# Kernel optimization log

Measured on AMD Instinct MI355X. Metric: run time of the kernel, lower is better.

The kernel has to match this reference:

```python
import jax, jax.numpy as jnp
import numpy as np

B = 16      # number of point clouds in the batch
N = 2048    # points per cloud
P = B * N   # total points (flat PyG-style batching)
K = 16      # neighbors per point (col 0 = self loop)
OUT = 512   # out_channels


def _linear(key, fi, fo):
    # torch nn.Linear default init: U(-1/sqrt(fi), 1/sqrt(fi))
    s = 1.0 / np.sqrt(fi)
    kw, kb = jax.random.split(key)
    W = jax.random.uniform(kw, (fi, fo), jnp.float32, -s, s)
    b = jax.random.uniform(kb, (fo,), jnp.float32, -s, s)
    return W, b


def setup_inputs() -> dict:
    key = jax.random.key(0)
    ks = jax.random.split(key, 6)
    pos = jax.random.normal(ks[0], (P, 3), jnp.float32)
    # flat batch vector: points are grouped contiguously per cloud
    batch = (jnp.arange(P, dtype=jnp.int32) // N).astype(jnp.int32)
    # within-cloud random neighbor indices (stand-in for knn/radius graph)
    base = (jnp.arange(P) // N) * N  # offset of each point's cloud
    nbr = base[:, None] + jax.random.randint(ks[1], (P, K), 0, N)
    nbr = nbr.at[:, 0].set(jnp.arange(P))  # self loop (PyG add_self_loops)
    W1, b1 = _linear(ks[2], 3, 64)          # sa1 MLP layer 1
    W2, b2 = _linear(ks[3], 64, 128)        # sa1 MLP layer 2
    W3, b3 = _linear(ks[4], 128 + 3, 256)   # sa2 MLP layer 1
    W4, b4 = _linear(ks[5], 256, OUT)       # sa2 MLP layer 2
    return dict(pos=pos, nbr=nbr.astype(jnp.int64), batch=batch,
                W1=W1, b1=b1, W2=W2, b2=b2, W3=W3, b3=b3, W4=W4, b4=b4)


def reference(pos, nbr, batch, W1, b1, W2, b2, W3, b3, W4, b4):
    # ----- sa1: x is None -> message = MLP(pos_j - pos_i), max-aggregated -----
    diff = pos[nbr] - pos[:, None, :]                      # [P, K, 3]
    h1 = jnp.maximum(diff @ W1 + b1, 0.0) @ W2 + b2        # [P, K, 128]
    x1 = jnp.max(h1, axis=1)                               # [P, 128]
    # ----- sa2: message = MLP([x1_j, pos_j - pos_i]), max-aggregated -----
    feats = jnp.concatenate([x1[nbr], diff], axis=-1)      # [P, K, 131]
    h2 = jnp.maximum(feats @ W3 + b3, 0.0) @ W4 + b4       # [P, K, 512]
    x2 = jnp.max(h2, axis=1)                               # [P, 512]
    # ----- global_max_pool over batch -----
    return jax.ops.segment_max(x2, batch, num_segments=B)  # [B, 512]
```

## Files before the change

kernel.cpp:

```cpp
#include <hip/hip_runtime.h>
#include <hip/hip_bf16.h>

#define PTOT   32768
#define KNB    16
#define NCLOUD 16
#define OUTC   512
#define A1S    168
#define A2S    264

typedef __attribute__((ext_vector_type(8)))  short v8bf;
typedef __attribute__((ext_vector_type(16))) float v16f;

__device__ __forceinline__ unsigned short f2b(float v) {
    __hip_bfloat16 h = __float2bfloat16(v);
    return *reinterpret_cast<unsigned short*>(&h);
}
__device__ __forceinline__ unsigned pk2(float a, float b) {
    return (unsigned)f2b(a) | ((unsigned)f2b(b) << 16);
}
__device__ __forceinline__ unsigned fenc(float f) {
    unsigned u = __float_as_uint(f);
    return (u & 0x80000000u) ? ~u : (u | 0x80000000u);
}
__device__ __forceinline__ float fdec(unsigned u) {
    unsigned b = (u & 0x80000000u) ? (u & 0x7FFFFFFFu) : ~u;
    return __uint_as_float(b);
}
__device__ __forceinline__ v16f zero16() {
    v16f z;
    #pragma unroll
    for (int i = 0; i < 16; ++i) z[i] = 0.0f;
    return z;
}

__global__ void prep_kernel(const float* __restrict__ W1, const float* __restrict__ W2,
                            const float* __restrict__ W3, const float* __restrict__ W4,
                            unsigned short* __restrict__ W1s, unsigned short* __restrict__ W2s,
                            unsigned short* __restrict__ W3s, unsigned short* __restrict__ W4s)
{
    int i = blockIdx.x * 256 + threadIdx.x;
    if (i < 40960) {
        int j = i & 7, n = (i >> 3) & 255, c2 = i >> 11;
        int k = c2 * 8 + j;
        W3s[i] = f2b(k < 131 ? W3[k * 256 + n] : 0.0f);
    }
    int i2 = i - 40960;
    if (i2 >= 0 && i2 < 131072) {
        int j = i2 & 7, n = (i2 >> 3) & 511, c2 = i2 >> 12;
        int k = c2 * 8 + j;
        W4s[i2] = f2b(W4[k * 512 + n]);
    }
    int i3 = i - 172032;
    if (i3 >= 0 && i3 < 1024) {
        int k = i3 & 15, n = i3 >> 4;
        W1s[i3] = f2b(k < 3 ? W1[k * 64 + n] : 0.0f);
    }
    int i4 = i - 173056;
    if (i4 >= 0 && i4 < 8192) {
        int k = i4 & 63, n = i4 >> 6;
        W2s[i4] = f2b(W2[k * 128 + n]);
    }
}

__global__ __launch_bounds__(256) void sa1_kernel(
    const float* __restrict__ pos, const int* __restrict__ nbr,
    const unsigned short* __restrict__ W1s, const float* __restrict__ b1,
    const unsigned short* __restrict__ W2s, const float* __restrict__ b2,
    unsigned short* __restrict__ x1b)
{
    __shared__ unsigned short A1d[64 * 16];
    __shared__ unsigned short A2[64 * 72];
    const int tid  = threadIdx.x;
    const int lane = tid & 63;
    const int wave = tid >> 6;
    const int l31  = lane & 31;
    const int h    = lane >> 5;
    const int p0   = blockIdx.x * 4;

    if (tid < 64) {
        int r = tid;
        int j = nbr[p0 * KNB + r];
        int p = p0 + (r >> 4);
        v8bf z;
        #pragma unroll
        for (int i = 0; i < 8; ++i) z[i] = 0;
        v8bf dv = z;
        dv[0] = (short)f2b(pos[j * 3 + 0] - pos[p * 3 + 0]);
        dv[1] = (short)f2b(pos[j * 3 + 1] - pos[p * 3 + 1]);
        dv[2] = (short)f2b(pos[j * 3 + 2] - pos[p * 3 + 2]);
        *(v8bf*)(A1d + r * 16)     = dv;
        *(v8bf*)(A1d + r * 16 + 8) = z;
    }
    const int c1 = (wave >> 1) * 32 + l31;
    v8bf b1f = *(const v8bf*)(W1s + c1 * 16 + h * 8);
    const float b1v = b1[c1];
    __syncthreads();

    {
        v8bf a = *(const v8bf*)(A1d + ((wave & 1) * 32 + l31) * 16 + h * 8);
        v16f acc = __builtin_amdgcn_mfma_f32_32x32x16_bf16(a, b1f, zero16(), 0, 0, 0);
        #pragma unroll
        for (int r = 0; r < 16; ++r) {
            int row = (wave & 1) * 32 + (r & 3) + 8 * (r >> 2) + 4 * h;
            A2[row * 72 + c1] = f2b(fmaxf(acc[r] + b1v, 0.0f));
        }
    }
    v8bf B2[4];
    #pragma unroll
    for (int kc = 0; kc < 4; ++kc)
        B2[kc] = *(const v8bf*)(W2s + (wave * 32 + l31) * 64 + kc * 16 + h * 8);
    const float b2v = b2[wave * 32 + l31];
    __syncthreads();

    #pragma unroll
    for (int rt = 0; rt < 2; ++rt) {
        v16f acc = zero16();
        #pragma unroll
        for (int kc = 0; kc < 4; ++kc) {
            v8bf a = *(const v8bf*)(A2 + (rt * 32 + l31) * 72 + kc * 16 + h * 8);
            acc = __builtin_amdgcn_mfma_f32_32x32x16_bf16(a, B2[kc], acc, 0, 0, 0);
        }
        float ma = acc[0], mb = acc[8];
        #pragma unroll
        for (int r = 1; r < 8; ++r) { ma = fmaxf(ma, acc[r]); mb = fmaxf(mb, acc[8 + r]); }
        ma = fmaxf(ma, __shfl_xor(ma, 32));
        mb = fmaxf(mb, __shfl_xor(mb, 32));
        int p = p0 + rt * 2 + h;
        float m = h ? mb : ma;
        x1b[p * 128 + wave * 32 + l31] = f2b(m + b2v);
    }
}

__global__ __launch_bounds__(256, 2) void sa2_kernel(
    const float* __restrict__ pos, const int* __restrict__ nbr,
    const int* __restrict__ batch,
    const unsigned short* __restrict__ W3s, const float* __restrict__ b3,
    const unsigned short* __restrict__ W4s, const float* __restrict__ b4,
    const unsigned short* __restrict__ x1b, unsigned* __restrict__ encbuf)
{
    __shared__ unsigned short S[64 * A2S];
    const int tid  = threadIdx.x;
    const int lane = tid & 63;
    const int wave = tid >> 6;
    const int l31  = lane & 31;
    const int h    = lane >> 5;
    const int p0   = blockIdx.x * 4;

    v8bf B1f[10];
    #pragma unroll
    for (int kc = 0; kc < 10; ++kc) {
        int c2 = kc * 2 + h;
        int n = (wave * 2) * 32 + l31;
        B1f[kc] = *(const v8bf*)(W3s + ((c2 * 256 + n) << 3));
    }
    const float b3v0 = b3[(wave * 2 + 0) * 32 + l31];
    const float b3v1 = b3[(wave * 2 + 1) * 32 + l31];

    {
        int r = tid >> 2, q4 = tid & 3;
        int j = nbr[p0 * KNB + r];
        const uint4* src = (const uint4*)(x1b + j * 128 + q4 * 32);
        uint4* dst = (uint4*)(S + r * A1S + q4 * 32);
        dst[0] = src[0]; dst[1] = src[1]; dst[2] = src[2]; dst[3] = src[3];
    }
    if (tid < 64) {
        int r = tid;
        int j = nbr[p0 * KNB + r];
        int p = p0 + (r >> 4);
        v8bf z;
        #pragma unroll
        for (int i = 0; i < 8; ++i) z[i] = 0;
        v8bf dv = z;
        dv[0] = (short)f2b(pos[j * 3 + 0] - pos[p * 3 + 0]);
        dv[1] = (short)f2b(pos[j * 3 + 1] - pos[p * 3 + 1]);
        dv[2] = (short)f2b(pos[j * 3 + 2] - pos[p * 3 + 2]);
        *(v8bf*)(S + r * A1S + 128) = dv;
        *(v8bf*)(S + r * A1S + 136) = z;
        *(v8bf*)(S + r * A1S + 144) = z;
        *(v8bf*)(S + r * A1S + 152) = z;
    }
    __syncthreads();

    unsigned st[2][16];
    #pragma unroll
    for (int ci = 0; ci < 2; ++ci) {
        if (ci == 1) {
            #pragma unroll
            for (int kc = 0; kc < 10; ++kc) {
                int c2 = kc * 2 + h;
                int n = (wave * 2 + 1) * 32 + l31;
                B1f[kc] = *(const v8bf*)(W3s + ((c2 * 256 + n) << 3));
            }
        }
        v16f acc0 = zero16(), acc1 = zero16();
        #pragma unroll
        for (int kc = 0; kc < 10; ++kc) {
            v8bf a0 = *(const v8bf*)(S + (l31)      * A1S + kc * 16 + h * 8);
            v8bf a1 = *(const v8bf*)(S + (32 + l31) * A1S + kc * 16 + h * 8);
            acc0 = __builtin_amdgcn_mfma_f32_32x32x16_bf16(a0, B1f[kc], acc0, 0, 0, 0);
            acc1 = __builtin_amdgcn_mfma_f32_32x32x16_bf16(a1, B1f[kc], acc1, 0, 0, 0);
        }
        float bv = ci ? b3v1 : b3v0;
        #pragma unroll
        for (int i = 0; i < 8; ++i) {
            st[ci][i]     = pk2(fmaxf(acc0[2 * i] + bv, 0.0f), fmaxf(acc0[2 * i + 1] + bv, 0.0f));
            st[ci][8 + i] = pk2(fmaxf(acc1[2 * i] + bv, 0.0f), fmaxf(acc1[2 * i + 1] + bv, 0.0f));
        }
    }
    __syncthreads();

    #pragma unroll
    for (int ci = 0; ci < 2; ++ci) {
        int c = (wave * 2 + ci) * 32 + l31;
        #pragma unroll
        for (int i = 0; i < 8; ++i) {
            int row = ((2 * i) & 3) + 8 * ((2 * i) >> 2) + 4 * h;
            S[row * A2S + c]            = (unsigned short)(st[ci][i] & 0xFFFF);
            S[(row + 1) * A2S + c]      = (unsigned short)(st[ci][i] >> 16);
            S[(32 + row) * A2S + c]     = (unsigned short)(st[ci][8 + i] & 0xFFFF);
            S[(32 + row + 1) * A2S + c] = (unsigned short)(st[ci][8 + i] >> 16);
        }
    }

    v8bf B2[16];
    {
        int n0 = (wave * 4) * 32 + l31;
        #pragma unroll
        for (int kc = 0; kc < 16; ++kc) {
            int c2 = kc * 2 + h;
            B2[kc] = *(const v8bf*)(W4s + ((c2 * 512 + n0) << 3));
        }
    }
    __syncthreads();

    const int cloud = batch[p0];
    #pragma unroll
    for (int ctp = 0; ctp < 4; ++ctp) {
        if (ctp > 0) {
            int n0 = (wave * 4 + ctp) * 32 + l31;
            #pragma unroll
            for (int kc = 0; kc < 16; ++kc) {
                int c2 = kc * 2 + h;
                B2[kc] = *(const v8bf*)(W4s + ((c2 * 512 + n0) << 3));
            }
        }
        v16f acc0 = zero16(), acc1 = zero16();
        #pragma unroll
        for (int kc = 0; kc < 16; ++kc) {
            v8bf a0 = *(const v8bf*)(S + (l31)      * A2S + kc * 16 + h * 8);
            v8bf a1 = *(const v8bf*)(S + (32 + l31) * A2S + kc * 16 + h * 8);
            acc0 = __builtin_amdgcn_mfma_f32_32x32x16_bf16(a0, B2[kc], acc0, 0, 0, 0);
            acc1 = __builtin_amdgcn_mfma_f32_32x32x16_bf16(a1, B2[kc], acc1, 0, 0, 0);
        }
        float m0 = acc0[0];
        #pragma unroll
        for (int r = 1; r < 16; ++r) m0 = fmaxf(m0, acc0[r]);
        #pragma unroll
        for (int r = 0; r < 16; ++r) m0 = fmaxf(m0, acc1[r]);
        m0 = fmaxf(m0, __shfl_xor(m0, 32));
        int ct = wave * 4 + ctp;
        m0 += b4[ct * 32 + l31];
        if (lane < 32) atomicMax(&encbuf[cloud * OUTC + ct * 32 + l31], fenc(m0));
    }
}

__global__ void finalize_kernel(const unsigned* __restrict__ encv,
                                float* __restrict__ out)
{
    int i = blockIdx.x * 256 + threadIdx.x;
    if (i < NCLOUD * OUTC) out[i] = fdec(encv[i]);
}

extern "C" void kernel_launch(void* const* d_in, const int* in_sizes, int n_in,
                              void* d_out, int out_size, void* d_ws, size_t ws_size,
                              hipStream_t stream)
{
    const float* pos   = (const float*)d_in[0];
    const int*   nbr   = (const int*)  d_in[1];
    const int*   batch = (const int*)  d_in[2];
    const float* W1    = (const float*)d_in[3];
    const float* b1    = (const float*)d_in[4];
    const float* W2    = (const float*)d_in[5];
    const float* b2    = (const float*)d_in[6];
    const float* W3    = (const float*)d_in[7];
    const float* b3    = (const float*)d_in[8];
    const float* W4    = (const float*)d_in[9];
    const float* b4    = (const float*)d_in[10];

    unsigned short* x1b = (unsigned short*)d_ws;
    unsigned short* W3s = (unsigned short*)((char*)d_ws + 8388608);
    unsigned short* W4s = (unsigned short*)((char*)d_ws + 8470528);
    unsigned*    encbuf = (unsigned*)((char*)d_ws + 8732672);
    unsigned short* W1s = (unsigned short*)((char*)d_ws + 8765440);
    unsigned short* W2s = (unsigned short*)((char*)d_ws + 8767488);

    hipMemsetAsync(encbuf, 0, NCLOUD * OUTC * sizeof(unsigned), stream);
    prep_kernel<<<708, 256, 0, stream>>>(W1, W2, W3, W4, W1s, W2s, W3s, W4s);
    sa1_kernel<<<PTOT / 4, 256, 0, stream>>>(pos, nbr, W1s, b1, W2s, b2, x1b);
    sa2_kernel<<<PTOT / 4, 256, 0, stream>>>(pos, nbr, batch, W3s, b3, W4s, b4, x1b, encbuf);
    finalize_kernel<<<(NCLOUD * OUTC + 255) / 256, 256, 0, stream>>>(encbuf, (float*)d_out);
}
```

Before: 292.3 us.

## Compute 2x2 MFMA tiles in sa2 with streamed weight fragments

Restructures both sa2 GEMM stages so each wave accumulates two column tiles at once. Every LDS A-fragment read now feeds four MFMAs, and weight fragments are loaded from global memory inside the K loop instead of being preloaded into register arrays. The first GEMM drops its last K chunk, which was entirely zero padding (131 real channels fit in 144). The launch-bounds occupancy hint is removed. The intent is fewer LDS reads, fewer MFMA instructions and lower register pressure, at the cost of weight-load latency now sitting inside the MFMA loop.

```diff
diff --git a/kernel.cpp b/kernel.cpp
--- a/kernel.cpp
+++ b/kernel.cpp
@@ -131,7 +131,7 @@
     }
 }
 
-__global__ __launch_bounds__(256, 2) void sa2_kernel(
+__global__ __launch_bounds__(256) void sa2_kernel(
     const float* __restrict__ pos, const int* __restrict__ nbr,
     const int* __restrict__ batch,
     const unsigned short* __restrict__ W3s, const float* __restrict__ b3,
@@ -146,13 +146,6 @@
     const int h    = lane >> 5;
     const int p0   = blockIdx.x * 4;
 
-    v8bf B1f[10];
-    #pragma unroll
-    for (int kc = 0; kc < 10; ++kc) {
-        int c2 = kc * 2 + h;
-        int n = (wave * 2) * 32 + l31;
-        B1f[kc] = *(const v8bf*)(W3s + ((c2 * 256 + n) << 3));
-    }
     const float b3v0 = b3[(wave * 2 + 0) * 32 + l31];
     const float b3v1 = b3[(wave * 2 + 1) * 32 + l31];
 
@@ -181,31 +174,28 @@
     }
     __syncthreads();
 
+    v16f g00 = zero16(), g01 = zero16(), g10 = zero16(), g11 = zero16();
+    const int n1a = (wave * 2 + 0) * 32 + l31;
+    const int n1b = (wave * 2 + 1) * 32 + l31;
+    #pragma unroll
+    for (int kc = 0; kc < 9; ++kc) {
+        v8bf a0 = *(const v8bf*)(S + (l31)      * A1S + kc * 16 + h * 8);
+        v8bf a1 = *(const v8bf*)(S + (32 + l31) * A1S + kc * 16 + h * 8);
+        int c2 = kc * 2 + h;
+        v8bf B0 = *(const v8bf*)(W3s + ((c2 * 256 + n1a) << 3));
+        v8bf B1 = *(const v8bf*)(W3s + ((c2 * 256 + n1b) << 3));
+        g00 = __builtin_amdgcn_mfma_f32_32x32x16_bf16(a0, B0, g00, 0, 0, 0);
+        g10 = __builtin_amdgcn_mfma_f32_32x32x16_bf16(a1, B0, g10, 0, 0, 0);
+        g01 = __builtin_amdgcn_mfma_f32_32x32x16_bf16(a0, B1, g01, 0, 0, 0);
+        g11 = __builtin_amdgcn_mfma_f32_32x32x16_bf16(a1, B1, g11, 0, 0, 0);
+    }
     unsigned st[2][16];
     #pragma unroll
-    for (int ci = 0; ci < 2; ++ci) {
-        if (ci == 1) {
-            #pragma unroll
-            for (int kc = 0; kc < 10; ++kc) {
-                int c2 = kc * 2 + h;
-                int n = (wave * 2 + 1) * 32 + l31;
-                B1f[kc] = *(const v8bf*)(W3s + ((c2 * 256 + n) << 3));
-            }
-        }
-        v16f acc0 = zero16(), acc1 = zero16();
-        #pragma unroll
-        for (int kc = 0; kc < 10; ++kc) {
-            v8bf a0 = *(const v8bf*)(S + (l31)      * A1S + kc * 16 + h * 8);
-            v8bf a1 = *(const v8bf*)(S + (32 + l31) * A1S + kc * 16 + h * 8);
-            acc0 = __builtin_amdgcn_mfma_f32_32x32x16_bf16(a0, B1f[kc], acc0, 0, 0, 0);
-            acc1 = __builtin_amdgcn_mfma_f32_32x32x16_bf16(a1, B1f[kc], acc1, 0, 0, 0);
-        }
-        float bv = ci ? b3v1 : b3v0;
-        #pragma unroll
-        for (int i = 0; i < 8; ++i) {
-            st[ci][i]     = pk2(fmaxf(acc0[2 * i] + bv, 0.0f), fmaxf(acc0[2 * i + 1] + bv, 0.0f));
-            st[ci][8 + i] = pk2(fmaxf(acc1[2 * i] + bv, 0.0f), fmaxf(acc1[2 * i + 1] + bv, 0.0f));
-        }
+    for (int i = 0; i < 8; ++i) {
+        st[0][i]     = pk2(fmaxf(g00[2 * i] + b3v0, 0.0f), fmaxf(g00[2 * i + 1] + b3v0, 0.0f));
+        st[0][8 + i] = pk2(fmaxf(g10[2 * i] + b3v0, 0.0f), fmaxf(g10[2 * i + 1] + b3v0, 0.0f));
+        st[1][i]     = pk2(fmaxf(g01[2 * i] + b3v1, 0.0f), fmaxf(g01[2 * i + 1] + b3v1, 0.0f));
+        st[1][8 + i] = pk2(fmaxf(g11[2 * i] + b3v1, 0.0f), fmaxf(g11[2 * i + 1] + b3v1, 0.0f));
     }
     __syncthreads();
 
@@ -221,46 +211,40 @@
             S[(32 + row + 1) * A2S + c] = (unsigned short)(st[ci][8 + i] >> 16);
         }
     }
-
-    v8bf B2[16];
-    {
-        int n0 = (wave * 4) * 32 + l31;
-        #pragma unroll
-        for (int kc = 0; kc < 16; ++kc) {
-            int c2 = kc * 2 + h;
-            B2[kc] = *(const v8bf*)(W4s + ((c2 * 512 + n0) << 3));
-        }
-    }
     __syncthreads();
 
     const int cloud = batch[p0];
     #pragma unroll
-    for (int ctp = 0; ctp < 4; ++ctp) {
-        if (ctp > 0) {
-            int n0 = (wave * 4 + ctp) * 32 + l31;
-            #pragma unroll
-            for (int kc = 0; kc < 16; ++kc) {
-                int c2 = kc * 2 + h;
-                B2[kc] = *(const v8bf*)(W4s + ((c2 * 512 + n0) << 3));
-            }
-        }
-        v16f acc0 = zero16(), acc1 = zero16();
+    for (int pass = 0; pass < 2; ++pass) {
+        const int ct0 = wave * 4 + pass * 2;
+        const int n0 = ct0 * 32 + l31;
+        const int n1 = (ct0 + 1) * 32 + l31;
+        v16f a00 = zero16(), a01 = zero16(), a10 = zero16(), a11 = zero16();
         #pragma unroll
         for (int kc = 0; kc < 16; ++kc) {
             v8bf a0 = *(const v8bf*)(S + (l31)      * A2S + kc * 16 + h * 8);
             v8bf a1 = *(const v8bf*)(S + (32 + l31) * A2S + kc * 16 + h * 8);
-            acc0 = __builtin_amdgcn_mfma_f32_32x32x16_bf16(a0, B2[kc], acc0, 0, 0, 0);
-            acc1 = __builtin_amdgcn_mfma_f32_32x32x16_bf16(a1, B2[kc], acc1, 0, 0, 0);
-        }
-        float m0 = acc0[0];
-        #pragma unroll
-        for (int r = 1; r < 16; ++r) m0 = fmaxf(m0, acc0[r]);
-        #pragma unroll
-        for (int r = 0; r < 16; ++r) m0 = fmaxf(m0, acc1[r]);
+            int c2 = kc * 2 + h;
+            v8bf Ba = *(const v8bf*)(W4s + ((c2 * 512 + n0) << 3));
+            v8bf Bb = *(const v8bf*)(W4s + ((c2 * 512 + n1) << 3));
+            a00 = __builtin_amdgcn_mfma_f32_32x32x16_bf16(a0, Ba, a00, 0, 0, 0);
+            a10 = __builtin_amdgcn_mfma_f32_32x32x16_bf16(a1, Ba, a10, 0, 0, 0);
+            a01 = __builtin_amdgcn_mfma_f32_32x32x16_bf16(a0, Bb, a01, 0, 0, 0);
+            a11 = __builtin_amdgcn_mfma_f32_32x32x16_bf16(a1, Bb, a11, 0, 0, 0);
+        }
+        float m0 = a00[0], m1 = a01[0];
+        #pragma unroll
+        for (int r = 1; r < 16; ++r) { m0 = fmaxf(m0, a00[r]); m1 = fmaxf(m1, a01[r]); }
+        #pragma unroll
+        for (int r = 0; r < 16; ++r) { m0 = fmaxf(m0, a10[r]); m1 = fmaxf(m1, a11[r]); }
         m0 = fmaxf(m0, __shfl_xor(m0, 32));
-        int ct = wave * 4 + ctp;
-        m0 += b4[ct * 32 + l31];
-        if (lane < 32) atomicMax(&encbuf[cloud * OUTC + ct * 32 + l31], fenc(m0));
+        m1 = fmaxf(m1, __shfl_xor(m1, 32));
+        m0 += b4[ct0 * 32 + l31];
+        m1 += b4[(ct0 + 1) * 32 + l31];
+        if (lane < 32) {
+            atomicMax(&encbuf[cloud * OUTC + ct0 * 32 + l31], fenc(m0));
+            atomicMax(&encbuf[cloud * OUTC + (ct0 + 1) * 32 + l31], fenc(m1));
+        }
     }
 }
 
```

Measured after the change: 288.1 us. Within noise of the previous version (-1.4%).
